# Optimization experiments

Measured on AMD Instinct MI355X. Metric: run time of the kernel, lower is better.

The kernel has to match this reference:

```python
import jax, jax.numpy as jnp
import numpy as np

EPS = 1e-5  # torch BatchNorm1d default eps
O, T, D, H1, H2 = 8, 4, 256, 64, 32


def setup_inputs() -> dict:
    key = jax.random.key(0)
    ks = jax.random.split(key, 8)
    B = 65536
    feature = jax.random.normal(ks[0], (B, D), dtype=jnp.float32)
    treatment = jax.random.randint(ks[1], (B,), 0, T, dtype=jnp.int64)
    s1 = 1.0 / np.sqrt(D)
    s2 = 1.0 / np.sqrt(H1)
    s3 = 1.0 / np.sqrt(H2)
    params = {
        # per (outcome, treatment) expert MLP weights
        'W1': jax.random.uniform(ks[2], (O, T, D, H1), jnp.float32, -s1, s1),
        'b1': jnp.zeros((O, T, H1), jnp.float32),
        'g1': jnp.ones((O, T, H1), jnp.float32),   # BN1 gamma
        'be1': jnp.zeros((O, T, H1), jnp.float32),  # BN1 beta
        'm1': jnp.zeros((O, T, H1), jnp.float32),   # BN1 running mean
        'v1': jnp.ones((O, T, H1), jnp.float32),    # BN1 running var
        'W2': jax.random.uniform(ks[3], (O, T, H1, H2), jnp.float32, -s2, s2),
        'b2': jnp.zeros((O, T, H2), jnp.float32),
        'g2': jnp.ones((O, T, H2), jnp.float32),
        'be2': jnp.zeros((O, T, H2), jnp.float32),
        'm2': jnp.zeros((O, T, H2), jnp.float32),
        'v2': jnp.ones((O, T, H2), jnp.float32),
        'W3': jax.random.uniform(ks[4], (O, T, H2), jnp.float32, -s3, s3),  # final Linear(32,1), squeezed
        'b3': jnp.zeros((O, T), jnp.float32),
    }
    return {'feature': feature, 'treatment': treatment, **params}


def _tlearner_fwd(x, t, W1, b1, g1, be1, m1, v1, W2, b2, g2, be2, m2, v2, W3, b3):
    # Dense evaluation of every (outcome, treatment) expert, then per-row
    # selection by treatment id. Equivalent (in eval mode: BN uses running
    # stats, dropout off) to the masked dispatch of the original module.
    h = jnp.einsum('bd,otdh->both', x, W1) + b1          # [B,O,T,H1]
    h = jax.nn.relu(h)
    h = (h - m1) * jax.lax.rsqrt(v1 + EPS) * g1 + be1    # BN1 (eval)
    h = jnp.einsum('both,othk->botk', h, W2) + b2        # [B,O,T,H2]
    h = jax.nn.relu(h)
    h = (h - m2) * jax.lax.rsqrt(v2 + EPS) * g2 + be2    # BN2 (eval)
    out = jnp.einsum('botk,otk->bot', h, W3) + b3        # [B,O,T]
    idx = t.astype(jnp.int32)[:, None, None]             # [B,1,1]
    return jnp.take_along_axis(out, jnp.broadcast_to(idx, (out.shape[0], O, 1)), axis=2)[..., 0]  # [B,O]


def reference(feature, treatment, W1, b1, g1, be1, m1, v1, W2, b2, g2, be2, m2, v2, W3, b3):
    return _tlearner_fwd(feature, treatment, W1, b1, g1, be1, m1, v1,
                         W2, b2, g2, be2, m2, v2, W3, b3)
```

## Files before the change

### kernel.cpp

```cpp
#include <hip/hip_runtime.h>
#include <cstdint>

typedef short bf16x8 __attribute__((ext_vector_type(8)));
typedef float f32x4 __attribute__((ext_vector_type(4)));

#define NO 8
#define NT 4
#define ND 256
#define NH1 64
#define NH2 32
#define BM 64
#define BNEPS 1e-5f

__device__ __forceinline__ unsigned bfpack2(float a, float b) {
    unsigned ua = __float_as_uint(a), ub = __float_as_uint(b);
    ua = (ua + 0x7FFFu + ((ua >> 16) & 1u)) >> 16;
    ub = (ub + 0x7FFFu + ((ub >> 16) & 1u)) >> 16;
    return ua | (ub << 16);
}


__global__ void k_init(int* __restrict__ ws, int* __restrict__ perm, int n) {
    const int gi = blockIdx.x * blockDim.x + threadIdx.x;
    if (gi < 16) ws[gi] = 0;
    if (gi < n) perm[gi] = -1;
}

__global__ void k_hist(const int* __restrict__ trt, int* __restrict__ cnt, int B) {
    __shared__ int loc[NT];
    const int tid = threadIdx.x;
    if (tid < NT) loc[tid] = 0;
    __syncthreads();
    const int i = blockIdx.x * blockDim.x + tid;
    if (i < B) atomicAdd(&loc[trt[i] & 3], 1);
    __syncthreads();
    if (tid < NT) atomicAdd(&cnt[tid], loc[tid]);
}

__global__ void k_prefix(int* __restrict__ ws) {
    int b = 0;
#pragma unroll
    for (int t = 0; t < NT; ++t) {
        ws[4 + t] = b; ws[12 + t] = b;
        b += (ws[t] + BM - 1) & ~(BM - 1);
    }
    ws[8] = b;
}

__global__ void k_scatter(const int* __restrict__ trt, int* __restrict__ ws,
                          int* __restrict__ perm, int B) {
    __shared__ int loc[NT], gb[NT];
    const int tid = threadIdx.x;
    if (tid < NT) loc[tid] = 0;
    __syncthreads();
    const int i = blockIdx.x * blockDim.x + tid;
    int tt = 0, pos = 0;
    if (i < B) { tt = trt[i] & 3; pos = atomicAdd(&loc[tt], 1); }
    __syncthreads();
    if (tid < NT) gb[tid] = atomicAdd(&ws[12 + tid], loc[tid]);
    __syncthreads();
    if (i < B) perm[gb[tt] + pos] = i;
}

__global__ __launch_bounds__(256) void k_prep(const float* __restrict__ W1,
                                              const float* __restrict__ W2,
                                              unsigned* __restrict__ W1T4,
                                              unsigned* __restrict__ W2T4) {
    const int bid = blockIdx.x, tid = threadIdx.x;
    if (bid < 256) {
        const int gi = bid * 256 + tid;
        const int lane = gi & 63, nt = (gi >> 6) & 31, c = (gi >> 11) & 7, t = gi >> 14;
        const int n16 = lane & 15, kg = lane >> 4;
        const int n = nt * 16 + n16, o = n >> 6, h = n & 63;
        const int k0 = c * 32 + kg * 8;
        const float* src = W1 + ((size_t)(o * NT + t) * ND + k0) * NH1 + h;
        float v[8];
#pragma unroll
        for (int j = 0; j < 8; ++j) v[j] = src[(size_t)j * NH1];
        uint4 q;
        q.x = bfpack2(v[0], v[1]); q.y = bfpack2(v[2], v[3]);
        q.z = bfpack2(v[4], v[5]); q.w = bfpack2(v[6], v[7]);
        ((uint4*)W1T4)[gi] = q;
    } else {
        const int gi = (bid - 256) * 256 + tid;
        const int m16 = gi & 15, kg = (gi >> 4) & 3, ks = (gi >> 6) & 1,
                  kt = (gi >> 7) & 1, o = (gi >> 8) & 7, t = gi >> 11;
        const int k2 = kt * 16 + m16, hb = ks * 32 + kg * 8;
        const float* src = W2 + ((size_t)(o * NT + t) * NH1 + hb) * NH2 + k2;
        float v[8];
#pragma unroll
        for (int j = 0; j < 8; ++j) v[j] = src[(size_t)j * NH2];
        uint4 q;
        q.x = bfpack2(v[0], v[1]); q.y = bfpack2(v[2], v[3]);
        q.z = bfpack2(v[4], v[5]); q.w = bfpack2(v[6], v[7]);
        ((uint4*)W2T4)[gi] = q;
    }
}

__global__ __launch_bounds__(256, 2) void k_main(
    const float* __restrict__ X, const int* __restrict__ ws, const int* __restrict__ perm,
    const unsigned short* __restrict__ W1T, const unsigned short* __restrict__ W2T,
    const float* __restrict__ pb1, const float* __restrict__ pg1, const float* __restrict__ pbe1,
    const float* __restrict__ pm1, const float* __restrict__ pv1,
    const float* __restrict__ pb2, const float* __restrict__ pg2, const float* __restrict__ pbe2,
    const float* __restrict__ pm2, const float* __restrict__ pv2,
    const float* __restrict__ W3, const float* __restrict__ pb3, float* __restrict__ out)
{
    const int m0 = blockIdx.x * BM;
    if (m0 >= ws[8]) return;
    const int t = (m0 >= ws[5]) + (m0 >= ws[6]) + (m0 >= ws[7]);
    const int tid = threadIdx.x;
    const int w = tid >> 6;
    const int l = tid & 63;

    __shared__ __align__(16) char LDS[65536];

    const int rid_reg = perm[m0 + l];

    {
        uint2 xr[16];
#pragma unroll
        for (int j = 0; j < 16; ++j) {
            const int rr = __shfl(rid_reg, w * 16 + j);
            const int rrow = rr < 0 ? 0 : rr;
            const float4 xv = *(const float4*)(X + (size_t)rrow * ND + l * 4);
            xr[j].x = bfpack2(xv.x, xv.y);
            xr[j].y = bfpack2(xv.z, xv.w);
        }
#pragma unroll
        for (int j = 0; j < 16; ++j) {
            const int r = w * 16 + j;
            *(uint2*)(LDS + r * 512 + ((l * 8) ^ ((r & 7) << 4))) = xr[j];
        }
    }

    f32x4 acc[8][4];
#pragma unroll
    for (int nt = 0; nt < 8; ++nt)
#pragma unroll
        for (int rt = 0; rt < 4; ++rt) acc[nt][rt] = (f32x4){0.f, 0.f, 0.f, 0.f};

    const char* W1Tt = (const char*)W1T + (size_t)t * 262144;
    const int ln4 = (l >> 4) * 4;

    __syncthreads();

#pragma unroll
    for (int c = 0; c < 8; ++c) {
        bf16x8 aA[8];
#pragma unroll
        for (int nt = 0; nt < 8; ++nt)
            aA[nt] = *(const bf16x8*)(W1Tt + c * 32768 + (w * 8 + nt) * 1024 + l * 16);
#pragma unroll
        for (int rt = 0; rt < 4; ++rt) {
            const int r = rt * 16 + (l & 15);
            const bf16x8 bX = *(const bf16x8*)(LDS + r * 512 +
                                               ((c * 64 + (l >> 4) * 16) ^ ((r & 7) << 4)));
#pragma unroll
            for (int nt = 0; nt < 8; ++nt)
                acc[nt][rt] = __builtin_amdgcn_mfma_f32_16x16x32_bf16(aA[nt], bX, acc[nt][rt], 0, 0, 0);
        }
    }
    __syncthreads();

#pragma unroll
    for (int nt = 0; nt < 8; ++nt) {
        const int n0 = (w * 8 + nt) * 16 + ln4;
        const int o = n0 >> 6, h0 = n0 & 63;
        const int pidx = (o * NT + t) * NH1 + h0;
        const float4 b1v = *(const float4*)(pb1 + pidx);
        const float4 g1v = *(const float4*)(pg1 + pidx);
        const float4 be1v = *(const float4*)(pbe1 + pidx);
        const float4 m1v = *(const float4*)(pm1 + pidx);
        const float4 v1v = *(const float4*)(pv1 + pidx);
        float bb[4], sc[4], sh[4];
        bb[0] = b1v.x; sc[0] = g1v.x * rsqrtf(v1v.x + BNEPS); sh[0] = be1v.x - m1v.x * sc[0];
        bb[1] = b1v.y; sc[1] = g1v.y * rsqrtf(v1v.y + BNEPS); sh[1] = be1v.y - m1v.y * sc[1];
        bb[2] = b1v.z; sc[2] = g1v.z * rsqrtf(v1v.z + BNEPS); sh[2] = be1v.z - m1v.z * sc[2];
        bb[3] = b1v.w; sc[3] = g1v.w * rsqrtf(v1v.w + BNEPS); sh[3] = be1v.w - m1v.w * sc[3];
#pragma unroll
        for (int rt = 0; rt < 4; ++rt) {
            const int r = rt * 16 + (l & 15);
            const f32x4 a = acc[nt][rt];
            const float z0 = fmaf(fmaxf(a[0] + bb[0], 0.f), sc[0], sh[0]);
            const float z1 = fmaf(fmaxf(a[1] + bb[1], 0.f), sc[1], sh[1]);
            const float z2 = fmaf(fmaxf(a[2] + bb[2], 0.f), sc[2], sh[2]);
            const float z3 = fmaf(fmaxf(a[3] + bb[3], 0.f), sc[3], sh[3]);
            uint2 pk;
            pk.x = bfpack2(z0, z1); pk.y = bfpack2(z2, z3);
            *(uint2*)(LDS + r * 1024 + (((unsigned)(n0 * 2)) ^ (unsigned)((r & 7) << 4))) = pk;
        }
    }

    bf16x8 aW[2][2][2];
#pragma unroll
    for (int oo = 0; oo < 2; ++oo) {
        const int o = w * 2 + oo;
#pragma unroll
        for (int kt = 0; kt < 2; ++kt)
#pragma unroll
            for (int ks = 0; ks < 2; ++ks)
                aW[oo][kt][ks] = *(const bf16x8*)((const char*)W2T +
                    ((((size_t)t * NO + o) * 2 + kt) * 2 + ks) * 1024 + l * 16);
    }
    f32x4 acc2[2][2][4];
#pragma unroll
    for (int oo = 0; oo < 2; ++oo)
#pragma unroll
        for (int kt = 0; kt < 2; ++kt)
#pragma unroll
            for (int rt2 = 0; rt2 < 4; ++rt2) acc2[oo][kt][rt2] = (f32x4){0.f, 0.f, 0.f, 0.f};

#pragma unroll
    for (int rt2 = 0; rt2 < 4; ++rt2) {
        const int r = rt2 * 16 + (l & 15);
        const unsigned swz = (unsigned)((r & 7) << 4);
#pragma unroll
        for (int ks = 0; ks < 2; ++ks) {
            const int nb = ks * 32 + (l >> 4) * 8;
#pragma unroll
            for (int oo = 0; oo < 2; ++oo) {
                const int n8 = (w * 2 + oo) * 64 + nb;
                const bf16x8 bH = *(const bf16x8*)(LDS + r * 1024 + (((unsigned)(n8 * 2)) ^ swz));
#pragma unroll
                for (int kt = 0; kt < 2; ++kt)
                    acc2[oo][kt][rt2] = __builtin_amdgcn_mfma_f32_16x16x32_bf16(aW[oo][kt][ks], bH, acc2[oo][kt][rt2], 0, 0, 0);
            }
        }
    }

    float p[2][4];
#pragma unroll
    for (int oo = 0; oo < 2; ++oo)
#pragma unroll
        for (int rt2 = 0; rt2 < 4; ++rt2) p[oo][rt2] = 0.f;

#pragma unroll
    for (int oo = 0; oo < 2; ++oo) {
        const int o = w * 2 + oo;
#pragma unroll
        for (int kt = 0; kt < 2; ++kt) {
            const int k2 = kt * 16 + ln4;
            const int pidx = (o * NT + t) * NH2 + k2;
            const float4 b2v = *(const float4*)(pb2 + pidx);
            const float4 g2v = *(const float4*)(pg2 + pidx);
            const float4 be2v = *(const float4*)(pbe2 + pidx);
            const float4 m2v = *(const float4*)(pm2 + pidx);
            const float4 v2v = *(const float4*)(pv2 + pidx);
            const float4 w3v = *(const float4*)(W3 + pidx);
            float bb[4], A3[4], C3[4];
            {
                const float s0 = g2v.x * rsqrtf(v2v.x + BNEPS);
                const float s1 = g2v.y * rsqrtf(v2v.y + BNEPS);
                const float s2 = g2v.z * rsqrtf(v2v.z + BNEPS);
                const float s3 = g2v.w * rsqrtf(v2v.w + BNEPS);
                bb[0] = b2v.x; A3[0] = s0 * w3v.x; C3[0] = (be2v.x - m2v.x * s0) * w3v.x;
                bb[1] = b2v.y; A3[1] = s1 * w3v.y; C3[1] = (be2v.y - m2v.y * s1) * w3v.y;
                bb[2] = b2v.z; A3[2] = s2 * w3v.z; C3[2] = (be2v.z - m2v.z * s2) * w3v.z;
                bb[3] = b2v.w; A3[3] = s3 * w3v.w; C3[3] = (be2v.w - m2v.w * s3) * w3v.w;
            }
#pragma unroll
            for (int rt2 = 0; rt2 < 4; ++rt2) {
                const f32x4 a = acc2[oo][kt][rt2];
                float s = fmaf(fmaxf(a[0] + bb[0], 0.f), A3[0], C3[0]);
                s = fmaf(fmaxf(a[1] + bb[1], 0.f), A3[1], s + C3[1]);
                s = fmaf(fmaxf(a[2] + bb[2], 0.f), A3[2], s + C3[2]);
                s = fmaf(fmaxf(a[3] + bb[3], 0.f), A3[3], s + C3[3]);
                p[oo][rt2] += s;
            }
        }
    }
#pragma unroll
    for (int oo = 0; oo < 2; ++oo)
#pragma unroll
        for (int rt2 = 0; rt2 < 4; ++rt2) {
            float v = p[oo][rt2];
            v += __shfl_xor(v, 16);
            v += __shfl_xor(v, 32);
            p[oo][rt2] = v;
        }

    const int oo_s = l >> 5;
    const int bsel = (l >> 4) & 1;
    const int o_s = w * 2 + oo_s;
    const float b3v = pb3[o_s * NT + t];
    const float v0 = oo_s ? (bsel ? p[1][1] : p[1][0]) : (bsel ? p[0][1] : p[0][0]);
    const float v1 = oo_s ? (bsel ? p[1][3] : p[1][2]) : (bsel ? p[0][3] : p[0][2]);
    const int rg0 = bsel * 16 + (l & 15);
    const int ra = __shfl(rid_reg, rg0);
    const int rb = __shfl(rid_reg, rg0 + 32);
    if (ra >= 0) out[(size_t)ra * NO + o_s] = v0 + b3v;
    if (rb >= 0) out[(size_t)rb * NO + o_s] = v1 + b3v;
}

extern "C" void kernel_launch(void* const* d_in, const int* in_sizes, int n_in,
                              void* d_out, int out_size, void* d_ws, size_t ws_size,
                              hipStream_t stream) {
    const float* X   = (const float*)d_in[0];
    const int* trt   = (const int*)d_in[1];
    const float* W1  = (const float*)d_in[2];
    const float* b1  = (const float*)d_in[3];
    const float* g1  = (const float*)d_in[4];
    const float* be1 = (const float*)d_in[5];
    const float* m1  = (const float*)d_in[6];
    const float* v1  = (const float*)d_in[7];
    const float* W2  = (const float*)d_in[8];
    const float* b2  = (const float*)d_in[9];
    const float* g2  = (const float*)d_in[10];
    const float* be2 = (const float*)d_in[11];
    const float* m2  = (const float*)d_in[12];
    const float* v2  = (const float*)d_in[13];
    const float* W3  = (const float*)d_in[14];
    const float* b3  = (const float*)d_in[15];
    float* out = (float*)d_out;

    const int B = in_sizes[1];
    const int permCap = B + NT * BM;
    int* wsi  = (int*)d_ws;
    int* perm = wsi + 16;
    char* wsb = (char*)d_ws;
    size_t off = 64 + (size_t)permCap * 4;
    off = (off + 15) & ~(size_t)15;
    unsigned* W1T4 = (unsigned*)(wsb + off);
    unsigned* W2T4 = (unsigned*)(wsb + off + 1048576);

    const int nb = (B + 255) / 256;
    const int nbi = (permCap + 255) / 256;
    k_init<<<nbi, 256, 0, stream>>>(wsi, perm, permCap);
    k_hist<<<nb, 256, 0, stream>>>(trt, wsi, B);
    k_prefix<<<1, 1, 0, stream>>>(wsi);
    k_scatter<<<nb, 256, 0, stream>>>(trt, wsi, perm, B);
    k_prep<<<288, 256, 0, stream>>>(W1, W2, W1T4, W2T4);

    const int gx = (B + NT * BM) / BM;
    k_main<<<gx, 256, 0, stream>>>(X, wsi, perm,
                                   (const unsigned short*)W1T4, (const unsigned short*)W2T4,
                                   b1, g1, be1, m1, v1, b2, g2, be2, m2, v2, W3, b3, out);
}
```

Baseline: 70.74 us.

## Fuse setup kernels, precompute BN params, halve row tile to 32

Merges init, histogram, prefix and weight-prep into one memset plus one combined kernel, and computes segment offsets inline in scatter and main, so the host launches fewer kernels. BN scale/shift and the W3-folded constants are precomputed once into small tables, which removes the per-block rsqrt work. The main kernel's row tile drops from 64 to 32 and occupancy is raised to 3 blocks per CU. Padding rows are now clamped to valid row indices instead of -1 sentinels. The cost is that each block re-reads the full W1 slice for half as many rows.

```diff
diff --git a/kernel.cpp b/kernel.cpp
--- a/kernel.cpp
+++ b/kernel.cpp
@@ -9,7 +9,7 @@
 #define ND 256
 #define NH1 64
 #define NH2 32
-#define BM 64
+#define BM 32
 #define BNEPS 1e-5f
 
 __device__ __forceinline__ unsigned bfpack2(float a, float b) {
@@ -20,55 +20,27 @@
 }
 
 
-__global__ void k_init(int* __restrict__ ws, int* __restrict__ perm, int n) {
-    const int gi = blockIdx.x * blockDim.x + threadIdx.x;
-    if (gi < 16) ws[gi] = 0;
-    if (gi < n) perm[gi] = -1;
-}
-
-__global__ void k_hist(const int* __restrict__ trt, int* __restrict__ cnt, int B) {
-    __shared__ int loc[NT];
-    const int tid = threadIdx.x;
-    if (tid < NT) loc[tid] = 0;
-    __syncthreads();
-    const int i = blockIdx.x * blockDim.x + tid;
-    if (i < B) atomicAdd(&loc[trt[i] & 3], 1);
-    __syncthreads();
-    if (tid < NT) atomicAdd(&cnt[tid], loc[tid]);
-}
-
-__global__ void k_prefix(int* __restrict__ ws) {
-    int b = 0;
-#pragma unroll
-    for (int t = 0; t < NT; ++t) {
-        ws[4 + t] = b; ws[12 + t] = b;
-        b += (ws[t] + BM - 1) & ~(BM - 1);
-    }
-    ws[8] = b;
-}
-
-__global__ void k_scatter(const int* __restrict__ trt, int* __restrict__ ws,
-                          int* __restrict__ perm, int B) {
-    __shared__ int loc[NT], gb[NT];
-    const int tid = threadIdx.x;
-    if (tid < NT) loc[tid] = 0;
-    __syncthreads();
-    const int i = blockIdx.x * blockDim.x + tid;
-    int tt = 0, pos = 0;
-    if (i < B) { tt = trt[i] & 3; pos = atomicAdd(&loc[tt], 1); }
-    __syncthreads();
-    if (tid < NT) gb[tid] = atomicAdd(&ws[12 + tid], loc[tid]);
-    __syncthreads();
-    if (i < B) perm[gb[tt] + pos] = i;
-}
-
-__global__ __launch_bounds__(256) void k_prep(const float* __restrict__ W1,
-                                              const float* __restrict__ W2,
-                                              unsigned* __restrict__ W1T4,
-                                              unsigned* __restrict__ W2T4) {
+__global__ void k_hist_prep(const int* __restrict__ trt, int* __restrict__ ws, int B,
+                            const float* __restrict__ W1, const float* __restrict__ W2,
+                            const float* __restrict__ b1, const float* __restrict__ g1,
+                            const float* __restrict__ be1, const float* __restrict__ m1,
+                            const float* __restrict__ v1,
+                            const float* __restrict__ b2, const float* __restrict__ g2,
+                            const float* __restrict__ be2, const float* __restrict__ m2,
+                            const float* __restrict__ v2, const float* __restrict__ W3,
+                            unsigned* __restrict__ W1T4, unsigned* __restrict__ W2T4,
+                            float* __restrict__ P1, float* __restrict__ P2) {
     const int bid = blockIdx.x, tid = threadIdx.x;
     if (bid < 256) {
-        const int gi = bid * 256 + tid;
+        __shared__ int loc[NT];
+        if (tid < NT) loc[tid] = 0;
+        __syncthreads();
+        const int i = bid * 256 + tid;
+        if (i < B) atomicAdd(&loc[trt[i] & 3], 1);
+        __syncthreads();
+        if (tid < NT) atomicAdd(&ws[tid], loc[tid]);
+    } else if (bid < 512) {
+        const int gi = (bid - 256) * 256 + tid;
         const int lane = gi & 63, nt = (gi >> 6) & 31, c = (gi >> 11) & 7, t = gi >> 14;
         const int n16 = lane & 15, kg = lane >> 4;
         const int n = nt * 16 + n16, o = n >> 6, h = n & 63;
@@ -81,8 +53,8 @@
         q.x = bfpack2(v[0], v[1]); q.y = bfpack2(v[2], v[3]);
         q.z = bfpack2(v[4], v[5]); q.w = bfpack2(v[6], v[7]);
         ((uint4*)W1T4)[gi] = q;
-    } else {
-        const int gi = (bid - 256) * 256 + tid;
+    } else if (bid < 544) {
+        const int gi = (bid - 512) * 256 + tid;
         const int m16 = gi & 15, kg = (gi >> 4) & 3, ks = (gi >> 6) & 1,
                   kt = (gi >> 7) & 1, o = (gi >> 8) & 7, t = gi >> 11;
         const int k2 = kt * 16 + m16, hb = ks * 32 + kg * 8;
@@ -94,53 +66,91 @@
         q.x = bfpack2(v[0], v[1]); q.y = bfpack2(v[2], v[3]);
         q.z = bfpack2(v[4], v[5]); q.w = bfpack2(v[6], v[7]);
         ((uint4*)W2T4)[gi] = q;
-    }
-}
-
-__global__ __launch_bounds__(256, 2) void k_main(
+    } else if (bid < 552) {
+        const int gi = (bid - 544) * 256 + tid;
+        const int t = gi >> 9, n = gi & 511;
+        const int o = n >> 6, h = n & 63;
+        const int idx = (o * NT + t) * NH1 + h;
+        const float sc = g1[idx] * rsqrtf(v1[idx] + BNEPS);
+        P1[gi] = sc;
+        P1[2048 + gi] = be1[idx] - m1[idx] * sc;
+        P1[4096 + gi] = b1[idx];
+    } else {
+        const int gi = (bid - 552) * 256 + tid;
+        const int t = gi >> 8, q = gi & 255;
+        const int o = q >> 5, k2 = q & 31;
+        const int idx = (o * NT + t) * NH2 + k2;
+        const float s = g2[idx] * rsqrtf(v2[idx] + BNEPS);
+        const float w3 = W3[idx];
+        P2[gi] = s * w3;
+        P2[1024 + gi] = (be2[idx] - m2[idx] * s) * w3;
+        P2[2048 + gi] = b2[idx];
+    }
+}
+
+__global__ void k_scatter(const int* __restrict__ trt, int* __restrict__ ws,
+                          int* __restrict__ perm, int B) {
+    __shared__ int loc[NT], gb[NT];
+    const int tid = threadIdx.x;
+    if (tid < NT) loc[tid] = 0;
+    __syncthreads();
+    const int i = blockIdx.x * blockDim.x + tid;
+    int tt = 0, pos = 0;
+    if (i < B) { tt = trt[i] & 3; pos = atomicAdd(&loc[tt], 1); }
+    __syncthreads();
+    if (tid < NT) {
+        const int c0 = ws[0], c1 = ws[1], c2 = ws[2];
+        const int ub = tid == 0 ? 0 : tid == 1 ? c0 : tid == 2 ? c0 + c1 : c0 + c1 + c2;
+        gb[tid] = ub + atomicAdd(&ws[4 + tid], loc[tid]);
+    }
+    __syncthreads();
+    if (i < B) perm[gb[tt] + pos] = i;
+}
+
+__global__ __launch_bounds__(256, 3) void k_main(
     const float* __restrict__ X, const int* __restrict__ ws, const int* __restrict__ perm,
-    const unsigned short* __restrict__ W1T, const unsigned short* __restrict__ W2T,
-    const float* __restrict__ pb1, const float* __restrict__ pg1, const float* __restrict__ pbe1,
-    const float* __restrict__ pm1, const float* __restrict__ pv1,
-    const float* __restrict__ pb2, const float* __restrict__ pg2, const float* __restrict__ pbe2,
-    const float* __restrict__ pm2, const float* __restrict__ pv2,
-    const float* __restrict__ W3, const float* __restrict__ pb3, float* __restrict__ out)
+    const char* __restrict__ W1T, const char* __restrict__ W2T,
+    const float* __restrict__ P1, const float* __restrict__ P2,
+    const float* __restrict__ pb3, float* __restrict__ out)
 {
+    const int c0 = ws[0], c1 = ws[1], c2 = ws[2], c3 = ws[3];
+    const int q0 = (c0 + 31) & ~31, q1 = (c1 + 31) & ~31, q2 = (c2 + 31) & ~31;
+    const int e0 = q0, e1 = q0 + q1, e2 = e1 + q2, e3 = e2 + ((c3 + 31) & ~31);
     const int m0 = blockIdx.x * BM;
-    if (m0 >= ws[8]) return;
-    const int t = (m0 >= ws[5]) + (m0 >= ws[6]) + (m0 >= ws[7]);
+    if (m0 >= e3) return;
+    const int t = (m0 >= e0) + (m0 >= e1) + (m0 >= e2);
+    const int pb = t == 0 ? 0 : t == 1 ? e0 : t == 2 ? e1 : e2;
+    const int ub = t == 0 ? 0 : t == 1 ? c0 : t == 2 ? c0 + c1 : c0 + c1 + c2;
+    const int n_t = t == 0 ? c0 : t == 1 ? c1 : t == 2 ? c2 : c3;
+    const int ploc0 = m0 - pb;
+
     const int tid = threadIdx.x;
     const int w = tid >> 6;
     const int l = tid & 63;
 
-    __shared__ __align__(16) char LDS[65536];
-
-    const int rid_reg = perm[m0 + l];
-
-    {
-        uint2 xr[16];
-#pragma unroll
-        for (int j = 0; j < 16; ++j) {
-            const int rr = __shfl(rid_reg, w * 16 + j);
-            const int rrow = rr < 0 ? 0 : rr;
-            const float4 xv = *(const float4*)(X + (size_t)rrow * ND + l * 4);
-            xr[j].x = bfpack2(xv.x, xv.y);
-            xr[j].y = bfpack2(xv.z, xv.w);
-        }
-#pragma unroll
-        for (int j = 0; j < 16; ++j) {
-            const int r = w * 16 + j;
-            *(uint2*)(LDS + r * 512 + ((l * 8) ^ ((r & 7) << 4))) = xr[j];
-        }
-    }
-
-    f32x4 acc[8][4];
+    __shared__ __align__(16) char LDS[32768];
+
+    const int pl = ploc0 + (l & 31);
+    const int rid_l = perm[ub + min(pl, n_t - 1)];
+
+#pragma unroll
+    for (int j = 0; j < 8; ++j) {
+        const int r = w * 8 + j;
+        const int rr = __shfl(rid_l, r);
+        const float4 xv = *(const float4*)(X + (size_t)rr * ND + l * 4);
+        uint2 pk;
+        pk.x = bfpack2(xv.x, xv.y);
+        pk.y = bfpack2(xv.z, xv.w);
+        *(uint2*)(LDS + r * 512 + ((l * 8) ^ ((r & 7) << 4))) = pk;
+    }
+
+    f32x4 acc[8][2];
 #pragma unroll
     for (int nt = 0; nt < 8; ++nt)
 #pragma unroll
-        for (int rt = 0; rt < 4; ++rt) acc[nt][rt] = (f32x4){0.f, 0.f, 0.f, 0.f};
-
-    const char* W1Tt = (const char*)W1T + (size_t)t * 262144;
+        for (int rt = 0; rt < 2; ++rt) acc[nt][rt] = (f32x4){0.f, 0.f, 0.f, 0.f};
+
+    const char* W1Tt = W1T + (size_t)t * 262144;
     const int ln4 = (l >> 4) * 4;
 
     __syncthreads();
@@ -152,7 +162,7 @@
         for (int nt = 0; nt < 8; ++nt)
             aA[nt] = *(const bf16x8*)(W1Tt + c * 32768 + (w * 8 + nt) * 1024 + l * 16);
 #pragma unroll
-        for (int rt = 0; rt < 4; ++rt) {
+        for (int rt = 0; rt < 2; ++rt) {
             const int r = rt * 16 + (l & 15);
             const bf16x8 bX = *(const bf16x8*)(LDS + r * 512 +
                                                ((c * 64 + (l >> 4) * 16) ^ ((r & 7) << 4)));
@@ -166,26 +176,18 @@
 #pragma unroll
     for (int nt = 0; nt < 8; ++nt) {
         const int n0 = (w * 8 + nt) * 16 + ln4;
-        const int o = n0 >> 6, h0 = n0 & 63;
-        const int pidx = (o * NT + t) * NH1 + h0;
-        const float4 b1v = *(const float4*)(pb1 + pidx);
-        const float4 g1v = *(const float4*)(pg1 + pidx);
-        const float4 be1v = *(const float4*)(pbe1 + pidx);
-        const float4 m1v = *(const float4*)(pm1 + pidx);
-        const float4 v1v = *(const float4*)(pv1 + pidx);
-        float bb[4], sc[4], sh[4];
-        bb[0] = b1v.x; sc[0] = g1v.x * rsqrtf(v1v.x + BNEPS); sh[0] = be1v.x - m1v.x * sc[0];
-        bb[1] = b1v.y; sc[1] = g1v.y * rsqrtf(v1v.y + BNEPS); sh[1] = be1v.y - m1v.y * sc[1];
-        bb[2] = b1v.z; sc[2] = g1v.z * rsqrtf(v1v.z + BNEPS); sh[2] = be1v.z - m1v.z * sc[2];
-        bb[3] = b1v.w; sc[3] = g1v.w * rsqrtf(v1v.w + BNEPS); sh[3] = be1v.w - m1v.w * sc[3];
-#pragma unroll
-        for (int rt = 0; rt < 4; ++rt) {
+        const int p = t * 512 + n0;
+        const float4 scv = *(const float4*)(P1 + p);
+        const float4 shv = *(const float4*)(P1 + 2048 + p);
+        const float4 bbv = *(const float4*)(P1 + 4096 + p);
+#pragma unroll
+        for (int rt = 0; rt < 2; ++rt) {
             const int r = rt * 16 + (l & 15);
             const f32x4 a = acc[nt][rt];
-            const float z0 = fmaf(fmaxf(a[0] + bb[0], 0.f), sc[0], sh[0]);
-            const float z1 = fmaf(fmaxf(a[1] + bb[1], 0.f), sc[1], sh[1]);
-            const float z2 = fmaf(fmaxf(a[2] + bb[2], 0.f), sc[2], sh[2]);
-            const float z3 = fmaf(fmaxf(a[3] + bb[3], 0.f), sc[3], sh[3]);
+            const float z0 = fmaf(fmaxf(a[0] + bbv.x, 0.f), scv.x, shv.x);
+            const float z1 = fmaf(fmaxf(a[1] + bbv.y, 0.f), scv.y, shv.y);
+            const float z2 = fmaf(fmaxf(a[2] + bbv.z, 0.f), scv.z, shv.z);
+            const float z3 = fmaf(fmaxf(a[3] + bbv.w, 0.f), scv.w, shv.w);
             uint2 pk;
             pk.x = bfpack2(z0, z1); pk.y = bfpack2(z2, z3);
             *(uint2*)(LDS + r * 1024 + (((unsigned)(n0 * 2)) ^ (unsigned)((r & 7) << 4))) = pk;
@@ -200,19 +202,19 @@
         for (int kt = 0; kt < 2; ++kt)
 #pragma unroll
             for (int ks = 0; ks < 2; ++ks)
-                aW[oo][kt][ks] = *(const bf16x8*)((const char*)W2T +
+                aW[oo][kt][ks] = *(const bf16x8*)(W2T +
                     ((((size_t)t * NO + o) * 2 + kt) * 2 + ks) * 1024 + l * 16);
     }
-    f32x4 acc2[2][2][4];
+    f32x4 acc2[2][2][2];
 #pragma unroll
     for (int oo = 0; oo < 2; ++oo)
 #pragma unroll
         for (int kt = 0; kt < 2; ++kt)
 #pragma unroll
-            for (int rt2 = 0; rt2 < 4; ++rt2) acc2[oo][kt][rt2] = (f32x4){0.f, 0.f, 0.f, 0.f};
-
-#pragma unroll
-    for (int rt2 = 0; rt2 < 4; ++rt2) {
+            for (int rt2 = 0; rt2 < 2; ++rt2) acc2[oo][kt][rt2] = (f32x4){0.f, 0.f, 0.f, 0.f};
+
+#pragma unroll
+    for (int rt2 = 0; rt2 < 2; ++rt2) {
         const int r = rt2 * 16 + (l & 15);
         const unsigned swz = (unsigned)((r & 7) << 4);
 #pragma unroll
@@ -229,43 +231,29 @@
         }
     }
 
-    float p[2][4];
+    float p[2][2];
 #pragma unroll
     for (int oo = 0; oo < 2; ++oo)
 #pragma unroll
-        for (int rt2 = 0; rt2 < 4; ++rt2) p[oo][rt2] = 0.f;
+        for (int rt2 = 0; rt2 < 2; ++rt2) p[oo][rt2] = 0.f;
 
 #pragma unroll
     for (int oo = 0; oo < 2; ++oo) {
         const int o = w * 2 + oo;
 #pragma unroll
         for (int kt = 0; kt < 2; ++kt) {
-            const int k2 = kt * 16 + ln4;
-            const int pidx = (o * NT + t) * NH2 + k2;
-            const float4 b2v = *(const float4*)(pb2 + pidx);
-            const float4 g2v = *(const float4*)(pg2 + pidx);
-            const float4 be2v = *(const float4*)(pbe2 + pidx);
-            const float4 m2v = *(const float4*)(pm2 + pidx);
-            const float4 v2v = *(const float4*)(pv2 + pidx);
-            const float4 w3v = *(const float4*)(W3 + pidx);
-            float bb[4], A3[4], C3[4];
-            {
-                const float s0 = g2v.x * rsqrtf(v2v.x + BNEPS);
-                const float s1 = g2v.y * rsqrtf(v2v.y + BNEPS);
-                const float s2 = g2v.z * rsqrtf(v2v.z + BNEPS);
-                const float s3 = g2v.w * rsqrtf(v2v.w + BNEPS);
-                bb[0] = b2v.x; A3[0] = s0 * w3v.x; C3[0] = (be2v.x - m2v.x * s0) * w3v.x;
-                bb[1] = b2v.y; A3[1] = s1 * w3v.y; C3[1] = (be2v.y - m2v.y * s1) * w3v.y;
-                bb[2] = b2v.z; A3[2] = s2 * w3v.z; C3[2] = (be2v.z - m2v.z * s2) * w3v.z;
-                bb[3] = b2v.w; A3[3] = s3 * w3v.w; C3[3] = (be2v.w - m2v.w * s3) * w3v.w;
-            }
-#pragma unroll
-            for (int rt2 = 0; rt2 < 4; ++rt2) {
+            const int q = o * 32 + kt * 16 + ln4;
+            const int p3 = t * 256 + q;
+            const float4 A3 = *(const float4*)(P2 + p3);
+            const float4 C3 = *(const float4*)(P2 + 1024 + p3);
+            const float4 bb = *(const float4*)(P2 + 2048 + p3);
+#pragma unroll
+            for (int rt2 = 0; rt2 < 2; ++rt2) {
                 const f32x4 a = acc2[oo][kt][rt2];
-                float s = fmaf(fmaxf(a[0] + bb[0], 0.f), A3[0], C3[0]);
-                s = fmaf(fmaxf(a[1] + bb[1], 0.f), A3[1], s + C3[1]);
-                s = fmaf(fmaxf(a[2] + bb[2], 0.f), A3[2], s + C3[2]);
-                s = fmaf(fmaxf(a[3] + bb[3], 0.f), A3[3], s + C3[3]);
+                float s = fmaf(fmaxf(a[0] + bb.x, 0.f), A3.x, C3.x);
+                s = fmaf(fmaxf(a[1] + bb.y, 0.f), A3.y, s + C3.y);
+                s = fmaf(fmaxf(a[2] + bb.z, 0.f), A3.z, s + C3.z);
+                s = fmaf(fmaxf(a[3] + bb.w, 0.f), A3.w, s + C3.w);
                 p[oo][rt2] += s;
             }
         }
@@ -273,7 +261,7 @@
 #pragma unroll
     for (int oo = 0; oo < 2; ++oo)
 #pragma unroll
-        for (int rt2 = 0; rt2 < 4; ++rt2) {
+        for (int rt2 = 0; rt2 < 2; ++rt2) {
             float v = p[oo][rt2];
             v += __shfl_xor(v, 16);
             v += __shfl_xor(v, 32);
@@ -281,16 +269,12 @@
         }
 
     const int oo_s = l >> 5;
-    const int bsel = (l >> 4) & 1;
+    const int rt2_s = (l >> 4) & 1;
     const int o_s = w * 2 + oo_s;
-    const float b3v = pb3[o_s * NT + t];
-    const float v0 = oo_s ? (bsel ? p[1][1] : p[1][0]) : (bsel ? p[0][1] : p[0][0]);
-    const float v1 = oo_s ? (bsel ? p[1][3] : p[1][2]) : (bsel ? p[0][3] : p[0][2]);
-    const int rg0 = bsel * 16 + (l & 15);
-    const int ra = __shfl(rid_reg, rg0);
-    const int rb = __shfl(rid_reg, rg0 + 32);
-    if (ra >= 0) out[(size_t)ra * NO + o_s] = v0 + b3v;
-    if (rb >= 0) out[(size_t)rb * NO + o_s] = v1 + b3v;
+    const int r = rt2_s * 16 + (l & 15);
+    const float v = oo_s ? (rt2_s ? p[1][1] : p[1][0]) : (rt2_s ? p[0][1] : p[0][0]);
+    const int ra = __shfl(rid_l, r);
+    if (ploc0 + r < n_t) out[(size_t)ra * NO + o_s] = v + pb3[o_s * NT + t];
 }
 
 extern "C" void kernel_launch(void* const* d_in, const int* in_sizes, int n_in,
@@ -315,25 +299,22 @@
     float* out = (float*)d_out;
 
     const int B = in_sizes[1];
-    const int permCap = B + NT * BM;
     int* wsi  = (int*)d_ws;
     int* perm = wsi + 16;
     char* wsb = (char*)d_ws;
-    size_t off = 64 + (size_t)permCap * 4;
-    off = (off + 15) & ~(size_t)15;
-    unsigned* W1T4 = (unsigned*)(wsb + off);
-    unsigned* W2T4 = (unsigned*)(wsb + off + 1048576);
-
-    const int nb = (B + 255) / 256;
-    const int nbi = (permCap + 255) / 256;
-    k_init<<<nbi, 256, 0, stream>>>(wsi, perm, permCap);
-    k_hist<<<nb, 256, 0, stream>>>(trt, wsi, B);
-    k_prefix<<<1, 1, 0, stream>>>(wsi);
-    k_scatter<<<nb, 256, 0, stream>>>(trt, wsi, perm, B);
-    k_prep<<<288, 256, 0, stream>>>(W1, W2, W1T4, W2T4);
-
-    const int gx = (B + NT * BM) / BM;
-    k_main<<<gx, 256, 0, stream>>>(X, wsi, perm,
-                                   (const unsigned short*)W1T4, (const unsigned short*)W2T4,
-                                   b1, g1, be1, m1, v1, b2, g2, be2, m2, v2, W3, b3, out);
-}
+    size_t off = (64 + (size_t)B * 4 + 15) & ~(size_t)15;
+    char* W1T = wsb + off;
+    char* W2T = W1T + 1048576;
+    float* P1 = (float*)(W2T + 131072);
+    float* P2 = P1 + 6144;
+
+    hipMemsetAsync(wsi, 0, 64, stream);
+    k_hist_prep<<<556, 256, 0, stream>>>(trt, wsi, B, W1, W2,
+                                         b1, g1, be1, m1, v1,
+                                         b2, g2, be2, m2, v2, W3,
+                                         (unsigned*)W1T, (unsigned*)W2T, P1, P2);
+    k_scatter<<<(B + 255) / 256, 256, 0, stream>>>(trt, wsi, perm, B);
+
+    const int gx = (B + 31) / 32 + 4;
+    k_main<<<gx, 256, 0, stream>>>(X, wsi, perm, W1T, W2T, P1, P2, b3, out);
+}
```

Result: faster. 61.82 us (-12.6%).
